# Optimization experiments

Hardware: AMD Instinct MI355X
Metric: run time of the kernel (lower is better)

## Reference

```python
import jax, jax.numpy as jnp
from jax import lax
import numpy as np

B, T, I, H, OUT = 4096, 168, 4, 64, 12


def setup_inputs() -> dict:
    key = jax.random.key(0)
    ks = jax.random.split(key, 14)
    s = 0.05
    return {
        "x": jax.random.normal(ks[0], (B, T, I), dtype=jnp.float32),
        # LSTM layer 0 (PyTorch gate order: i, f, g, o)
        "Wih0": jax.random.normal(ks[1], (4 * H, I), dtype=jnp.float32) * s,
        "Whh0": jax.random.normal(ks[2], (4 * H, H), dtype=jnp.float32) * s,
        "bih0": jax.random.normal(ks[3], (4 * H,), dtype=jnp.float32) * s,
        "bhh0": jax.random.normal(ks[4], (4 * H,), dtype=jnp.float32) * s,
        # LSTM layer 1
        "Wih1": jax.random.normal(ks[5], (4 * H, H), dtype=jnp.float32) * s,
        "Whh1": jax.random.normal(ks[6], (4 * H, H), dtype=jnp.float32) * s,
        "bih1": jax.random.normal(ks[7], (4 * H,), dtype=jnp.float32) * s,
        "bhh1": jax.random.normal(ks[8], (4 * H,), dtype=jnp.float32) * s,
        # FC head: Linear(64,64) -> ReLU -> Linear(64,12)
        "W1": jax.random.normal(ks[9], (64, H), dtype=jnp.float32) * s,
        "b1": jax.random.normal(ks[10], (64,), dtype=jnp.float32) * s,
        "W2": jax.random.normal(ks[11], (OUT, 64), dtype=jnp.float32) * s,
        "b2": jax.random.normal(ks[12], (OUT,), dtype=jnp.float32) * s,
    }


def _lstm_layer(x, Wih, Whh, bih, bhh):
    # x: [B, T, in]; returns hidden sequence [B, T, H]
    Bsz = x.shape[0]
    Hd = Whh.shape[1]
    # Precompute input contribution for all timesteps: [B, T, 4H]
    xg = jnp.einsum('bti,gi->btg', x, Wih) + bih + bhh

    def step(carry, xg_t):
        h, c = carry
        g = xg_t + h @ Whh.T  # [B, 4H]
        i, f, gg, o = jnp.split(g, 4, axis=-1)
        i = jax.nn.sigmoid(i)
        f = jax.nn.sigmoid(f)
        gg = jnp.tanh(gg)
        o = jax.nn.sigmoid(o)
        c = f * c + i * gg
        h = o * jnp.tanh(c)
        return (h, c), h

    h0 = jnp.zeros((Bsz, Hd), x.dtype)
    (_, _), hs = lax.scan(step, (h0, h0), jnp.swapaxes(xg, 0, 1))  # hs: [T, B, H]
    return jnp.swapaxes(hs, 0, 1)


def reference(x, Wih0, Whh0, bih0, bhh0, Wih1, Whh1, bih1, bhh1, W1, b1, W2, b2):
    # Eval-mode forward: dropout layers are identity.
    h1 = _lstm_layer(x, Wih0, Whh0, bih0, bhh0)   # [B, T, H]
    h2 = _lstm_layer(h1, Wih1, Whh1, bih1, bhh1)  # [B, T, H]
    last = h2[:, -1, :]                            # [B, H]
    z = jax.nn.relu(last @ W1.T + b1)              # [B, 64]
    out = z @ W2.T + b2                            # [B, 12]
    return out.reshape(-1, 3, 4)
```

## Files before the change

### kernel.cpp

```cpp
#include <hip/hip_runtime.h>


typedef _Float16 h8 __attribute__((ext_vector_type(8)));
typedef _Float16 h4 __attribute__((ext_vector_type(4)));
typedef float f4 __attribute__((ext_vector_type(4)));

#define ROWB 208
#define HBUF (16 * ROWB)
#define XTAB_OFF 0
#define XTAB_BYTES (169 * 256)
#define H0_OFF XTAB_BYTES
#define H1_OFF (H0_OFF + 2 * HBUF)
#define SMEM_TOTAL (H1_OFF + 2 * HBUF)

#define K1F 1.4426950408889634f
#define K2F 2.8853900817779268f

__device__ __forceinline__ float exp2_(float x) {
#if __has_builtin(__builtin_amdgcn_exp2f)
  return __builtin_amdgcn_exp2f(x);
#else
  float r; asm("v_exp_f32 %0, %1" : "=v"(r) : "v"(x)); return r;
#endif
}
__device__ __forceinline__ float rcp_(float x) {
#if __has_builtin(__builtin_amdgcn_rcpf)
  return __builtin_amdgcn_rcpf(x);
#else
  float r; asm("v_rcp_f32 %0, %1" : "=v"(r) : "v"(x)); return r;
#endif
}

__device__ __forceinline__ f4 mfma16(h8 a, h8 b, f4 c) {
  return __builtin_amdgcn_mfma_f32_16x16x32_f16(a, b, c, 0, 0, 0);
}

__device__ __forceinline__ h8 load_w8s(const float* __restrict__ p, float sc) {
  h8 r;
#pragma unroll
  for (int j = 0; j < 8; j++) r[j] = (_Float16)(p[j] * sc);
  return r;
}

__device__ __forceinline__ void lstm_act_s(float gi, float gf, float gg, float go,
                                           float& c, float& h) {
  float Ei = exp2_(-gi);
  float Ef = exp2_(-gf);
  float Eg = exp2_(gg);
  float Eo = exp2_(-go);
  float A = 1.f + Ei, B = 1.f + Ef, C = 1.f + Eg, D = 1.f + Eo;
  float AB = A * B, CD = C * D, BD = B * D;
  float R  = rcp_(AB * CD);
  float fv = (A * CD) * R;
  float ig = (BD * (Eg - 1.f)) * R;
  float ov = (AB * C) * R;
  c = fv * c + ig;
  float r2 = rcp_(exp2_(c * K2F) + 1.f);
  h = ov * (1.f - 2.f * r2);
}

extern "C" __global__ void __launch_bounds__(512, 2)
weather_lstm_mfma10(const float* __restrict__ x,
                    const float* __restrict__ Wih0, const float* __restrict__ Whh0,
                    const float* __restrict__ bih0, const float* __restrict__ bhh0,
                    const float* __restrict__ Wih1, const float* __restrict__ Whh1,
                    const float* __restrict__ bih1, const float* __restrict__ bhh1,
                    const float* __restrict__ W1, const float* __restrict__ b1,
                    const float* __restrict__ W2, const float* __restrict__ b2,
                    float* __restrict__ out)
{
  __shared__ __align__(16) unsigned char smem[SMEM_TOTAL];
  const int tid  = threadIdx.x;
  const int lane = tid & 63;
  const int w    = tid >> 6;
  const int col  = lane & 15;
  const int quad = lane >> 4;
  const bool isL0 = (w < 4);
  const int wl   = w & 3;
  const int u0   = wl * 16;
  const int uu   = u0 + quad * 4;
  const int sB   = blockIdx.x * 16;

  h8 wfrag[16];
  f4 bias[4];
#pragma unroll
  for (int g = 0; g < 4; ++g) {
    const float sc = (g == 2) ? K2F : K1F;
    const int r = g * 64 + u0 + col;
    if (isL0) {
#pragma unroll
      for (int f = 0; f < 2; ++f)
        wfrag[2 * g + f] = load_w8s(Whh0 + r * 64 + f * 32 + quad * 8, sc);
      h8 xw = {};
      if (quad == 0) {
#pragma unroll
        for (int j = 0; j < 4; ++j) xw[j] = (_Float16)(Wih0[r * 4 + j] * sc);
      }
      wfrag[8 + g] = xw;
#pragma unroll
      for (int j = 0; j < 4; ++j)
        bias[g][j] = (bih0[g * 64 + uu + j] + bhh0[g * 64 + uu + j]) * sc;
    } else {
#pragma unroll
      for (int f = 0; f < 2; ++f) {
        wfrag[2 * g + f]     = load_w8s(Wih1 + r * 64 + f * 32 + quad * 8, sc);
        wfrag[8 + 2 * g + f] = load_w8s(Whh1 + r * 64 + f * 32 + quad * 8, sc);
      }
#pragma unroll
      for (int j = 0; j < 4; ++j)
        bias[g][j] = (bih1[g * 64 + uu + j] + bhh1[g * 64 + uu + j]) * sc;
    }
  }

  for (int idx = tid; idx < SMEM_TOTAL / 4; idx += 512) ((int*)smem)[idx] = 0;
  __syncthreads();
  for (int idx = tid; idx < 16 * 168; idx += 512) {
    const int c_ = idx / 168, t_ = idx - c_ * 168;
    f4 xv = *(const f4*)(x + ((size_t)(sB + c_) * 168 + t_) * 4);
    h4 xh;
#pragma unroll
    for (int j = 0; j < 4; j++) xh[j] = (_Float16)xv[j];
    *(h4*)(smem + XTAB_OFF + t_ * 256 + c_ * 16) = xh;
  }
  __syncthreads();

  f4 acc[4];
  float cst[4] = {0.f, 0.f, 0.f, 0.f};
  float hl[4]  = {0.f, 0.f, 0.f, 0.f};
  const int bo = col * ROWB + quad * 16;
  const int wo = col * ROWB + uu * 2;
  const unsigned char* xp = smem + XTAB_OFF + col * 16;

  for (int k = 0; k <= 169; ++k) {
    const int sl = k & 1, slp = sl ^ 1;

    if (isL0) {
      if (k <= 167) {
        const unsigned char* h0r = smem + H0_OFF + slp * HBUF;
        h8 b0  = *(const h8*)(h0r + bo);
        h8 b1v = *(const h8*)(h0r + bo + 64);
        h8 bx  = *(const h8*)(xp + k * 256);
#pragma unroll
        for (int g = 0; g < 4; ++g) acc[g] = mfma16(wfrag[2 * g], b0, bias[g]);
#pragma unroll
        for (int g = 0; g < 4; ++g) acc[g] = mfma16(wfrag[2 * g + 1], b1v, acc[g]);
#pragma unroll
        for (int g = 0; g < 4; ++g) acc[g] = mfma16(wfrag[8 + g], bx, acc[g]);
      }
    } else {
      if (k >= 2) {
        h4 hv;
#pragma unroll
        for (int a = 0; a < 4; ++a) {
          float ho;
          lstm_act_s(acc[0][a], acc[1][a], acc[2][a], acc[3][a], cst[a], ho);
          hl[a] = ho;
          hv[a] = (_Float16)ho;
        }
        *(h4*)(smem + H1_OFF + sl * HBUF + wo) = hv;
      }
    }
    __syncthreads();

    if (isL0) {
      if (k <= 167) {
        h4 hv;
#pragma unroll
        for (int a = 0; a < 4; ++a) {
          float ho;
          lstm_act_s(acc[0][a], acc[1][a], acc[2][a], acc[3][a], cst[a], ho);
          hv[a] = (_Float16)ho;
        }
        *(h4*)(smem + H0_OFF + sl * HBUF + wo) = hv;
      }
    } else {
      if (k >= 1 && k <= 168) {
        const unsigned char* h0r = smem + H0_OFF + slp * HBUF;
        const unsigned char* h1r = smem + H1_OFF + sl * HBUF;
        h8 b0  = *(const h8*)(h0r + bo);
        h8 b1v = *(const h8*)(h0r + bo + 64);
        h8 q0  = *(const h8*)(h1r + bo);
        h8 q1  = *(const h8*)(h1r + bo + 64);
#pragma unroll
        for (int g = 0; g < 4; ++g) acc[g] = mfma16(wfrag[2 * g], b0, bias[g]);
#pragma unroll
        for (int g = 0; g < 4; ++g) acc[g] = mfma16(wfrag[2 * g + 1], b1v, acc[g]);
#pragma unroll
        for (int g = 0; g < 4; ++g) acc[g] = mfma16(wfrag[8 + 2 * g], q0, acc[g]);
#pragma unroll
        for (int g = 0; g < 4; ++g) acc[g] = mfma16(wfrag[9 + 2 * g], q1, acc[g]);
      }
    }
    __syncthreads();
  }

  float* fh = (float*)smem;
  if (!isL0) {
    f4 hv; hv[0] = hl[0]; hv[1] = hl[1]; hv[2] = hl[2]; hv[3] = hl[3];
    *(f4*)(fh + col * 64 + uu) = hv;
  }
  __syncthreads();

  {
    const int u = tid & 63, g2 = tid >> 6;
    const float* w1r = W1 + u * 64;
    float* zl = (float*)(smem + 4096);
#pragma unroll
    for (int rep = 0; rep < 2; ++rep) {
      const int s2 = g2 + rep * 8;
      float za = b1[u];
      const float* f0 = fh + s2 * 64;
      for (int j = 0; j < 64; ++j) za += w1r[j] * f0[j];
      zl[s2 * 64 + u] = fmaxf(za, 0.f);
    }
  }
  __syncthreads();

  if (tid < 192) {
    const float* zl = (const float*)(smem + 4096);
    const int s2 = tid / 12, o = tid - s2 * 12;
    float a = b2[o];
    for (int j = 0; j < 64; ++j) a += W2[o * 64 + j] * zl[s2 * 64 + j];
    out[(sB + s2) * 12 + o] = a;
  }
}

extern "C" void kernel_launch(void* const* d_in, const int* in_sizes, int n_in,
                              void* d_out, int out_size, void* d_ws, size_t ws_size,
                              hipStream_t stream) {
  (void)in_sizes; (void)n_in; (void)d_ws; (void)ws_size; (void)out_size;
  const float* x    = (const float*)d_in[0];
  const float* Wih0 = (const float*)d_in[1];
  const float* Whh0 = (const float*)d_in[2];
  const float* bih0 = (const float*)d_in[3];
  const float* bhh0 = (const float*)d_in[4];
  const float* Wih1 = (const float*)d_in[5];
  const float* Whh1 = (const float*)d_in[6];
  const float* bih1 = (const float*)d_in[7];
  const float* bhh1 = (const float*)d_in[8];
  const float* W1   = (const float*)d_in[9];
  const float* b1   = (const float*)d_in[10];
  const float* W2   = (const float*)d_in[11];
  const float* b2   = (const float*)d_in[12];

  weather_lstm_mfma10<<<dim3(256), dim3(512), 0, stream>>>(
      x, Wih0, Whh0, bih0, bhh0, Wih1, Whh1, bih1, bhh1, W1, b1, W2, b2,
      (float*)d_out);
}
```

Before: 242.0 us.

## Stream x per step from global and interleave layer roles across SIMDs

Removes the per-block LDS staging table for the input sequence and instead prefetches the next timestep's x values from global memory into registers one step ahead. This shrinks shared memory per block from about 70KB to about 13KB, which may allow more blocks per CU. It also remaps the waves so layer-0 and layer-1 roles alternate across wave indices, which can spread the two roles more evenly over the SIMDs. The price is a global load on the serial recurrence path every step, with its latency hidden only by a one-step prefetch.

```diff
diff --git a/kernel.cpp b/kernel.cpp
--- a/kernel.cpp
+++ b/kernel.cpp
@@ -7,11 +7,9 @@
 
 #define ROWB 208
 #define HBUF (16 * ROWB)
-#define XTAB_OFF 0
-#define XTAB_BYTES (169 * 256)
-#define H0_OFF XTAB_BYTES
-#define H1_OFF (H0_OFF + 2 * HBUF)
-#define SMEM_TOTAL (H1_OFF + 2 * HBUF)
+#define H0_OFF 0
+#define H1_OFF (2 * HBUF)
+#define SMEM_TOTAL (4 * HBUF)
 
 #define K1F 1.4426950408889634f
 #define K2F 2.8853900817779268f
@@ -60,7 +58,7 @@
 }
 
 extern "C" __global__ void __launch_bounds__(512, 2)
-weather_lstm_mfma10(const float* __restrict__ x,
+weather_lstm_mfma12(const float* __restrict__ x,
                     const float* __restrict__ Wih0, const float* __restrict__ Whh0,
                     const float* __restrict__ bih0, const float* __restrict__ bhh0,
                     const float* __restrict__ Wih1, const float* __restrict__ Whh1,
@@ -75,8 +73,10 @@
   const int w    = tid >> 6;
   const int col  = lane & 15;
   const int quad = lane >> 4;
-  const bool isL0 = (w < 4);
-  const int wl   = w & 3;
+  const int role = (w ^ (w >> 2)) & 1;
+  const bool isL0 = (role == 0);
+  const int adj  = (w >= 4) ? ((w & 1) ? -1 : 1) : 0;
+  const int wl   = (w + adj) >> 1;
   const int u0   = wl * 16;
   const int uu   = u0 + quad * 4;
   const int sB   = blockIdx.x * 16;
@@ -114,22 +114,16 @@
 
   for (int idx = tid; idx < SMEM_TOTAL / 4; idx += 512) ((int*)smem)[idx] = 0;
   __syncthreads();
-  for (int idx = tid; idx < 16 * 168; idx += 512) {
-    const int c_ = idx / 168, t_ = idx - c_ * 168;
-    f4 xv = *(const f4*)(x + ((size_t)(sB + c_) * 168 + t_) * 4);
-    h4 xh;
-#pragma unroll
-    for (int j = 0; j < 4; j++) xh[j] = (_Float16)xv[j];
-    *(h4*)(smem + XTAB_OFF + t_ * 256 + c_ * 16) = xh;
-  }
-  __syncthreads();
+
+  f4 xc = {};
+  if (isL0 && quad == 0)
+    xc = *(const f4*)(x + ((size_t)(sB + col) * 168 + 0) * 4);
 
   f4 acc[4];
   float cst[4] = {0.f, 0.f, 0.f, 0.f};
   float hl[4]  = {0.f, 0.f, 0.f, 0.f};
   const int bo = col * ROWB + quad * 16;
   const int wo = col * ROWB + uu * 2;
-  const unsigned char* xp = smem + XTAB_OFF + col * 16;
 
   for (int k = 0; k <= 169; ++k) {
     const int sl = k & 1, slp = sl ^ 1;
@@ -139,7 +133,18 @@
         const unsigned char* h0r = smem + H0_OFF + slp * HBUF;
         h8 b0  = *(const h8*)(h0r + bo);
         h8 b1v = *(const h8*)(h0r + bo + 64);
-        h8 bx  = *(const h8*)(xp + k * 256);
+        h8 bx = {};
+        if (quad == 0) {
+#pragma unroll
+          for (int j = 0; j < 4; ++j) bx[j] = (_Float16)xc[j];
+        }
+        {
+          const int kn = (k < 167) ? k + 1 : k;
+          f4 xn = xc;
+          if (quad == 0)
+            xn = *(const f4*)(x + ((size_t)(sB + col) * 168 + kn) * 4);
+          xc = xn;
+        }
 #pragma unroll
         for (int g = 0; g < 4; ++g) acc[g] = mfma16(wfrag[2 * g], b0, bias[g]);
 #pragma unroll
@@ -243,7 +248,7 @@
   const float* W2   = (const float*)d_in[11];
   const float* b2   = (const float*)d_in[12];
 
-  weather_lstm_mfma10<<<dim3(256), dim3(512), 0, stream>>>(
+  weather_lstm_mfma12<<<dim3(256), dim3(512), 0, stream>>>(
       x, Wih0, Whh0, bih0, bhh0, Wih1, Whh1, bih1, bhh1, W1, b1, W2, b2,
       (float*)d_out);
 }
```

Result: no change. 238.9 us (-1.3%).
